# Kernel tuning notes

Hardware: AMD Instinct MI355X
Metric: run time of the kernel (lower is better)

## Reference

```python
import jax, jax.numpy as jnp
import numpy as np

CONF_THRES = 0.96
IOU_THRES = 0.45
MAX_CAND = 2048        # fixed candidate cap (jit-static stand-in for data-dependent nonzero)
DET_PER_IMG = 300
AGNOSTIC = False
LABEL_OFF = 4.0        # class offset for batched NMS; boxes lie within [-0.5, 1.5]


def _cxcywh_to_xyxy(b):
    cx, cy, w, h = b[..., 0], b[..., 1], b[..., 2], b[..., 3]
    return jnp.stack([cx - 0.5 * w, cy - 0.5 * h, cx + 0.5 * w, cy + 0.5 * h], axis=-1)


def _box_iou(a, b):
    # a: [K,4], b: [K,4] -> [K,K]
    lt = jnp.maximum(a[:, None, :2], b[None, :, :2])
    rb = jnp.minimum(a[:, None, 2:], b[None, :, 2:])
    wh = jnp.clip(rb - lt, 0.0)
    inter = wh[..., 0] * wh[..., 1]
    area_a = (a[:, 2] - a[:, 0]) * (a[:, 3] - a[:, 1])
    area_b = (b[:, 2] - b[:, 0]) * (b[:, 3] - b[:, 1])
    return inter / (area_a[:, None] + area_b[None, :] - inter + 1e-9)


def _process_image(x, nc):
    # x: [N, 5+nc]
    obj = x[:, 4]
    cls_scores = x[:, 5:] * obj[:, None]                 # x[:,5:] *= x[:,4:5]
    boxes = _cxcywh_to_xyxy(x[:, :4])                    # [N,4]
    # multi-label candidates: (obj > conf) pre-filter, then (obj*cls > conf)
    cand_mask = (cls_scores > CONF_THRES) & (obj[:, None] > CONF_THRES)
    flat_scores = jnp.where(cand_mask, cls_scores, -1.0).reshape(-1)  # [N*nc]
    top_scores, top_idx = jax.lax.top_k(flat_scores, MAX_CAND)        # sorted desc
    anchor = top_idx // nc
    label = top_idx % nc
    cand_boxes = boxes[anchor]                           # [K,4]
    valid = top_scores > 0.0

    # batched (class-aware) NMS via per-class coordinate offset
    if AGNOSTIC:
        nms_boxes = cand_boxes
    else:
        nms_boxes = cand_boxes + (label.astype(cand_boxes.dtype) * LABEL_OFF)[:, None]
    iou = _box_iou(nms_boxes, nms_boxes)                 # [K,K]
    idxs = jnp.arange(MAX_CAND)

    def body(i, keep):
        suppress = keep[i] & (iou[i] > IOU_THRES) & (idxs > i)
        return keep & ~suppress

    keep = jax.lax.fori_loop(0, MAX_CAND, body, valid)
    kept_scores = jnp.where(keep, top_scores, -1.0)
    det_scores, det_idx = jax.lax.top_k(kept_scores, DET_PER_IMG)
    det_valid = det_scores > 0.0
    det = jnp.concatenate(
        [cand_boxes[det_idx], det_scores[:, None], label[det_idx].astype(x.dtype)[:, None]],
        axis=1,
    )  # [DET_PER_IMG, 6] = (x1, y1, x2, y2, score, class)
    return jnp.where(det_valid[:, None], det, 0.0)


def setup_inputs() -> dict:
    key = jax.random.key(0)
    prediction = jax.random.uniform(key, (8, 25200, 85), dtype=jnp.float32)
    return {"prediction": prediction}


def reference(prediction):
    nc = prediction.shape[2] - 5
    return jax.vmap(lambda x: _process_image(x, nc))(prediction)
```

## Files before the change

kernel.cpp:

```cpp
#include <hip/hip_runtime.h>
#include <stdint.h>

#define CONF 0.96f
#define IOUT 0.45f
#define NA 25200
#define DIM 85
#define NC 80
#define NIMG 8
#define NCAND 2048
#define CAPRAW 4096
#define NDET 300
#define CSTRIDE 32

__global__ void k0_zero(int* __restrict__ cnt) {
    cnt[threadIdx.x] = 0;
}

#define APB 112
#define BCAP 256
__global__ __launch_bounds__(256) void k1_filter(
    const float* __restrict__ pred, int* __restrict__ cnt,
    float* __restrict__ raw_s, int* __restrict__ raw_f) {
    __shared__ float lds[APB * DIM];
    __shared__ float l_s[BCAP];
    __shared__ int   l_f[BCAP];
    __shared__ int   l_cnt, l_base;
    int tid = threadIdx.x;
    int img = blockIdx.y;
    int a0 = blockIdx.x * APB;
    if (tid == 0) l_cnt = 0;

    const float4* src = (const float4*)(pred + ((size_t)img * NA + a0) * DIM);
    float4* dst = (float4*)lds;
    for (int i = tid; i < (APB * DIM / 4); i += 256) dst[i] = src[i];
    __syncthreads();

    for (int it = 0; it < (APB * NC / 256); ++it) {
        int w = tid + it * 256;
        int al = w / NC;
        int c = w - al * NC;
        float obj = lds[al * DIM + 4];
        float s = lds[al * DIM + 5 + c] * obj;
        if (s > CONF && obj > CONF) {
            int p = atomicAdd(&l_cnt, 1);
            if (p < BCAP) { l_s[p] = s; l_f[p] = (a0 + al) * NC + c; }
        }
    }
    __syncthreads();
    int c = l_cnt; if (c > BCAP) c = BCAP;
    if (tid == 0) l_base = c ? atomicAdd(&cnt[img * CSTRIDE], c) : 0;
    __syncthreads();
    int base = l_base;
    for (int i = tid; i < c; i += 256) {
        int pos = base + i;
        if (pos < CAPRAW) {
            raw_s[img * CAPRAW + pos] = l_s[i];
            raw_f[img * CAPRAW + pos] = l_f[i];
        }
    }
}

__global__ __launch_bounds__(1024) void k2_sort(
    const float* __restrict__ pred,
    const int* __restrict__ cnt, int* __restrict__ n_arr,
    const float* __restrict__ raw_s, const int* __restrict__ raw_f,
    float* __restrict__ score, int* __restrict__ label,
    float* __restrict__ ox1, float* __restrict__ oy1,
    float* __restrict__ ox2, float* __restrict__ oy2,
    float* __restrict__ area,
    float* __restrict__ rx1, float* __restrict__ ry1,
    float* __restrict__ rx2, float* __restrict__ ry2) {
    __shared__ uint64_t key[CAPRAW];
    int img = blockIdx.x;
    int tid = threadIdx.x;
    int m = cnt[img * CSTRIDE]; if (m > CAPRAW) m = CAPRAW;
    for (int i = tid; i < CAPRAW; i += 1024) {
        uint64_t k = 0;
        if (i < m) {
            float s = raw_s[img * CAPRAW + i];
            uint32_t f = (uint32_t)raw_f[img * CAPRAW + i];
            k = ((uint64_t)__float_as_uint(s) << 32) | (uint32_t)(~f);
        }
        key[i] = k;
    }
    __syncthreads();
    for (unsigned kk = 2; kk <= CAPRAW; kk <<= 1) {
        for (unsigned j = kk >> 1; j > 0; j >>= 1) {
            for (unsigned i = tid; i < CAPRAW; i += 1024) {
                unsigned ixj = i ^ j;
                if (ixj > i) {
                    uint64_t x = key[i], y = key[ixj];
                    bool up = ((i & kk) == 0);
                    bool sw = up ? (x < y) : (x > y);
                    if (sw) { key[i] = y; key[ixj] = x; }
                }
            }
            __syncthreads();
        }
    }
    int n = m; if (n > NCAND) n = NCAND;
    if (tid == 0) n_arr[img] = n;
    for (int jj = tid; jj < n; jj += 1024) {
        uint64_t k = key[jj];
        float s = __uint_as_float((uint32_t)(k >> 32));
        uint32_t f = ~((uint32_t)k);
        int anchor = (int)(f / NC);
        int lab = (int)(f - (uint32_t)anchor * NC);
        const float* p = pred + ((size_t)img * NA + anchor) * DIM;
        float cx = p[0], cy = p[1], wv = p[2], hv = p[3];
        float x1 = cx - 0.5f * wv, y1 = cy - 0.5f * hv;
        float x2 = cx + 0.5f * wv, y2 = cy + 0.5f * hv;
        float off = (float)lab * 4.0f;
        size_t o = (size_t)img * NCAND + jj;
        score[o] = s; label[o] = lab;
        rx1[o] = x1; ry1[o] = y1; rx2[o] = x2; ry2[o] = y2;
        float o1 = x1 + off, o2 = y1 + off, o3 = x2 + off, o4 = y2 + off;
        ox1[o] = o1; oy1[o] = o2; ox2[o] = o3; oy2[o] = o4;
        area[o] = (o3 - o1) * (o4 - o2);
    }
}

__global__ void k3_mask(const int* __restrict__ n_arr,
                        const float* __restrict__ ox1, const float* __restrict__ oy1,
                        const float* __restrict__ ox2, const float* __restrict__ oy2,
                        const float* __restrict__ area, uint32_t* __restrict__ mask) {
    int img = blockIdx.y;
    int i = blockIdx.x;
    int n = n_arr[img];
    int lane = threadIdx.x;
    size_t base = (size_t)img * NCAND;
    uint32_t word = 0;
    if (i < n) {
        float ax1 = ox1[base + i], ay1 = oy1[base + i];
        float ax2 = ox2[base + i], ay2 = oy2[base + i];
        float aar = area[base + i];
        for (int b = 0; b < 32; ++b) {
            int j = lane + (b << 6);
            if (j < n && j > i) {
                float bx1 = ox1[base + j], by1 = oy1[base + j];
                float bx2 = ox2[base + j], by2 = oy2[base + j];
                float bar = area[base + j];
                float ltx = fmaxf(ax1, bx1), lty = fmaxf(ay1, by1);
                float rbx = fminf(ax2, bx2), rby = fminf(ay2, by2);
                float wv = fmaxf(rbx - ltx, 0.0f), hv = fmaxf(rby - lty, 0.0f);
                float inter = wv * hv;
                float iou = inter / (aar + bar - inter + 1e-9f);
                if (iou > IOUT) word |= (1u << b);
            }
        }
    }
    mask[((size_t)img * NCAND + i) * 64 + lane] = word;
}

__global__ void k4_scan(const int* __restrict__ n_arr,
                        const uint32_t* __restrict__ mask,
                        const float* __restrict__ score, const int* __restrict__ label,
                        const float* __restrict__ rx1, const float* __restrict__ ry1,
                        const float* __restrict__ rx2, const float* __restrict__ ry2,
                        float* __restrict__ out) {
    int img = blockIdx.x;
    int lane = threadIdx.x;
    int n = n_arr[img];
    size_t cbase = (size_t)img * NCAND;
    const uint32_t* rowp = mask + cbase * 64 + lane;
    float* outp = out + (size_t)img * NDET * 6;

    uint32_t removed = 0;
    int kcnt = 0;
    constexpr int PF = 32;
    uint32_t buf[PF];
#pragma unroll
    for (int k = 0; k < PF; ++k) buf[k] = rowp[(size_t)k * 64];
    for (int ib = 0; ib < n; ib += PF) {
#pragma unroll
        for (int k = 0; k < PF; ++k) {
            int i = ib + k;
            uint32_t row = buf[k];
            int pi = i + PF; if (pi > NCAND - 1) pi = NCAND - 1;
            buf[k] = rowp[(size_t)pi * 64];
            uint32_t w = (uint32_t)__builtin_amdgcn_readlane((int)removed, i & 63);
            uint32_t kept = ((w >> (i >> 6)) & 1u) ^ 1u;
            kcnt += (int)kept;
            removed |= row & (0u - kept);
        }
        if (kcnt >= NDET) break;
    }

    int bsum = 0;
    for (int b = 0; b < 32; ++b) {
        int j = lane + (b << 6);
        bool kept = (j < n) && (((removed >> b) & 1u) == 0u);
        unsigned long long m64 = __ballot(kept);
        if (kept) {
            int r = bsum + (int)__popcll(m64 & ((1ull << lane) - 1ull));
            if (r < NDET) {
                float* o = outp + (size_t)r * 6;
                o[0] = rx1[cbase + j]; o[1] = ry1[cbase + j];
                o[2] = rx2[cbase + j]; o[3] = ry2[cbase + j];
                o[4] = score[cbase + j]; o[5] = (float)label[cbase + j];
            }
        }
        bsum += (int)__popcll(m64);
        if (bsum >= NDET) break;
    }
    int nk = bsum < NDET ? bsum : NDET;
    for (int idx = nk * 6 + lane; idx < NDET * 6; idx += 64) outp[idx] = 0.0f;
}

extern "C" void kernel_launch(void* const* d_in, const int* in_sizes, int n_in,
                              void* d_out, int out_size, void* d_ws, size_t ws_size,
                              hipStream_t stream) {
    const float* pred = (const float*)d_in[0];
    float* out = (float*)d_out;
    char* w = (char*)d_ws;

    const size_t A_CNT = 0;
    const size_t A_N   = 1024;
    const size_t A_RS  = 1280;
    const size_t SZ_RAW = (size_t)NIMG * CAPRAW * 4;
    const size_t A_RF  = A_RS + SZ_RAW;
    const size_t SA    = A_RF + SZ_RAW;
    const size_t SZ_S  = (size_t)NIMG * NCAND * 4;

    int*   cnt   = (int*)(w + A_CNT);
    int*   n_arr = (int*)(w + A_N);
    float* raw_s = (float*)(w + A_RS);
    int*   raw_f = (int*)(w + A_RF);
    float* score = (float*)(w + SA + 0 * SZ_S);
    int*   label = (int*)(w + SA + 1 * SZ_S);
    float* ox1   = (float*)(w + SA + 2 * SZ_S);
    float* oy1   = (float*)(w + SA + 3 * SZ_S);
    float* ox2   = (float*)(w + SA + 4 * SZ_S);
    float* oy2   = (float*)(w + SA + 5 * SZ_S);
    float* area  = (float*)(w + SA + 6 * SZ_S);
    float* rx1   = (float*)(w + SA + 7 * SZ_S);
    float* ry1   = (float*)(w + SA + 8 * SZ_S);
    float* rx2   = (float*)(w + SA + 9 * SZ_S);
    float* ry2   = (float*)(w + SA + 10 * SZ_S);
    uint32_t* mask = (uint32_t*)(w + SA + 11 * SZ_S);

    k0_zero<<<1, NIMG * CSTRIDE, 0, stream>>>(cnt);
    dim3 g1(NA / APB, NIMG);
    k1_filter<<<g1, 256, 0, stream>>>(pred, cnt, raw_s, raw_f);
    k2_sort<<<NIMG, 1024, 0, stream>>>(pred, cnt, n_arr, raw_s, raw_f,
        score, label, ox1, oy1, ox2, oy2, area, rx1, ry1, rx2, ry2);
    dim3 g3(NCAND, NIMG);
    k3_mask<<<g3, 64, 0, stream>>>(n_arr, ox1, oy1, ox2, oy2, area, mask);
    k4_scan<<<NIMG, 64, 0, stream>>>(n_arr, mask, score, label,
        rx1, ry1, rx2, ry2, out);
}
```

Baseline: 196.3 us.

## Replace single-block bitonic sort with parallel rank-by-counting scatter

Swaps the per-image 1024-thread bitonic sort over 4096 keys in shared memory for a counting rank. Each candidate counts how many keys beat it and scatters itself directly to its sorted slot. Work is spread across up to 64 wavefront blocks per image, with wavefront readlane broadcasts and prefetching of the next tile. This removes the many barrier-separated bitonic passes run on only 8 blocks, but costs O(m^2) comparisons per image, which grows with the candidate count.

Result: faster. 183.4 us (-6.6%).

```diff
diff --git a/kernel.cpp b/kernel.cpp
--- a/kernel.cpp
+++ b/kernel.cpp
@@ -60,7 +60,7 @@
     }
 }
 
-__global__ __launch_bounds__(1024) void k2_sort(
+__global__ __launch_bounds__(64) void k2_rank(
     const float* __restrict__ pred,
     const int* __restrict__ cnt, int* __restrict__ n_arr,
     const float* __restrict__ raw_s, const int* __restrict__ raw_f,
@@ -70,48 +70,58 @@
     float* __restrict__ area,
     float* __restrict__ rx1, float* __restrict__ ry1,
     float* __restrict__ rx2, float* __restrict__ ry2) {
-    __shared__ uint64_t key[CAPRAW];
-    int img = blockIdx.x;
-    int tid = threadIdx.x;
+    int img = blockIdx.y;
+    int lane = threadIdx.x;
     int m = cnt[img * CSTRIDE]; if (m > CAPRAW) m = CAPRAW;
-    for (int i = tid; i < CAPRAW; i += 1024) {
-        uint64_t k = 0;
-        if (i < m) {
-            float s = raw_s[img * CAPRAW + i];
-            uint32_t f = (uint32_t)raw_f[img * CAPRAW + i];
-            k = ((uint64_t)__float_as_uint(s) << 32) | (uint32_t)(~f);
-        }
-        key[i] = k;
-    }
-    __syncthreads();
-    for (unsigned kk = 2; kk <= CAPRAW; kk <<= 1) {
-        for (unsigned j = kk >> 1; j > 0; j >>= 1) {
-            for (unsigned i = tid; i < CAPRAW; i += 1024) {
-                unsigned ixj = i ^ j;
-                if (ixj > i) {
-                    uint64_t x = key[i], y = key[ixj];
-                    bool up = ((i & kk) == 0);
-                    bool sw = up ? (x < y) : (x > y);
-                    if (sw) { key[i] = y; key[ixj] = x; }
-                }
-            }
-            __syncthreads();
-        }
-    }
-    int n = m; if (n > NCAND) n = NCAND;
-    if (tid == 0) n_arr[img] = n;
-    for (int jj = tid; jj < n; jj += 1024) {
-        uint64_t k = key[jj];
-        float s = __uint_as_float((uint32_t)(k >> 32));
-        uint32_t f = ~((uint32_t)k);
-        int anchor = (int)(f / NC);
-        int lab = (int)(f - (uint32_t)anchor * NC);
+    if (blockIdx.x == 0 && lane == 0) n_arr[img] = m < NCAND ? m : NCAND;
+    int idx = blockIdx.x * 64 + lane;
+    if (blockIdx.x * 64 >= m) return;
+
+    const float* rs = raw_s + img * CAPRAW;
+    const int*   rf = raw_f + img * CAPRAW;
+    bool valid = idx < m;
+    uint64_t my = 0;
+    uint32_t myf = 0;
+    if (valid) {
+        float s = rs[idx];
+        myf = (uint32_t)rf[idx];
+        my = ((uint64_t)__float_as_uint(s) << 32) | (uint32_t)(~myf);
+    }
+
+    int ntile = (m + 63) >> 6;
+    uint64_t cur = 0;
+    {
+        int j = lane;
+        if (j < m) cur = ((uint64_t)__float_as_uint(rs[j]) << 32) | (uint32_t)(~(uint32_t)rf[j]);
+    }
+    int rank = 0;
+    for (int t = 0; t < ntile; ++t) {
+        uint64_t nxt = 0;
+        int jn = ((t + 1) << 6) + lane;
+        if (t + 1 < ntile && jn < m)
+            nxt = ((uint64_t)__float_as_uint(rs[jn]) << 32) | (uint32_t)(~(uint32_t)rf[jn]);
+        int tlo = (int)(uint32_t)cur;
+        int thi = (int)(uint32_t)(cur >> 32);
+#pragma unroll 16
+        for (int i = 0; i < 64; ++i) {
+            uint32_t blo = (uint32_t)__builtin_amdgcn_readlane(tlo, i);
+            uint32_t bhi = (uint32_t)__builtin_amdgcn_readlane(thi, i);
+            uint64_t bk = ((uint64_t)bhi << 32) | blo;
+            rank += (bk > my) ? 1 : 0;
+        }
+        cur = nxt;
+    }
+
+    if (valid && rank < NCAND) {
+        float s = __uint_as_float((uint32_t)(my >> 32));
+        int anchor = (int)(myf / NC);
+        int lab = (int)(myf - (uint32_t)anchor * NC);
         const float* p = pred + ((size_t)img * NA + anchor) * DIM;
         float cx = p[0], cy = p[1], wv = p[2], hv = p[3];
         float x1 = cx - 0.5f * wv, y1 = cy - 0.5f * hv;
         float x2 = cx + 0.5f * wv, y2 = cy + 0.5f * hv;
         float off = (float)lab * 4.0f;
-        size_t o = (size_t)img * NCAND + jj;
+        size_t o = (size_t)img * NCAND + rank;
         score[o] = s; label[o] = lab;
         rx1[o] = x1; ry1[o] = y1; rx2[o] = x2; ry2[o] = y2;
         float o1 = x1 + off, o2 = y1 + off, o3 = x2 + off, o4 = y2 + off;
@@ -242,7 +252,8 @@
     k0_zero<<<1, NIMG * CSTRIDE, 0, stream>>>(cnt);
     dim3 g1(NA / APB, NIMG);
     k1_filter<<<g1, 256, 0, stream>>>(pred, cnt, raw_s, raw_f);
-    k2_sort<<<NIMG, 1024, 0, stream>>>(pred, cnt, n_arr, raw_s, raw_f,
+    dim3 g2(CAPRAW / 64, NIMG);
+    k2_rank<<<g2, 64, 0, stream>>>(pred, cnt, n_arr, raw_s, raw_f,
         score, label, ox1, oy1, ox2, oy2, area, rx1, ry1, rx2, ry2);
     dim3 g3(NCAND, NIMG);
     k3_mask<<<g3, 64, 0, stream>>>(n_arr, ox1, oy1, ox2, oy2, area, mask);
```
